# Performance work log

Measured on AMD Instinct MI355X. Metric: run time of the kernel, lower is better.

Reference implementation:

```python
import jax, jax.numpy as jnp
import numpy as np

T, N, E, D, H, L = 8, 50000, 800000, 128, 128, 2


def setup_inputs() -> dict:
    key = jax.random.key(0)
    ks = jax.random.split(key, 16)
    s = 1.0 / np.sqrt(H)  # glorot-ish scale so gates don't saturate
    inp = {
        "x": jax.random.normal(ks[0], (T, N, D), jnp.float32),
        "h0": jax.random.normal(ks[1], (L, N, H), jnp.float32) * 0.1,
        "edge_index": jax.random.randint(ks[2], (2, E), 0, N, jnp.int32),
    }
    for j, n in enumerate(["Wxz", "Whz", "Wxr", "Whr", "Wxh", "Whh"]):
        inp[n] = jax.random.normal(ks[3 + j], (L, H, H), jnp.float32) * s
    for n in ["bxz", "bhz", "bxr", "bhr", "bxh", "bhh"]:
        inp[n] = jnp.zeros((L, H), jnp.float32)
    return inp


def reference(x, h0, Wxz, Whz, Wxr, Whr, Wxh, Whh,
              bxz, bhz, bxr, bhr, bxh, bhh, edge_index):
    n_nodes = x.shape[1]
    n_layer = h0.shape[0]
    # GCNConv(improved=True): add self-loops with weight 2, symmetric norm.
    loop = jnp.arange(n_nodes, dtype=edge_index.dtype)
    row = jnp.concatenate([edge_index[0], loop])
    col = jnp.concatenate([edge_index[1], loop])
    w = jnp.concatenate([jnp.ones((edge_index.shape[1],), x.dtype),
                         jnp.full((n_nodes,), 2.0, x.dtype)])
    deg = jax.ops.segment_sum(w, row, num_segments=n_nodes)
    dinv = jnp.where(deg > 0, deg ** -0.5, 0.0)
    norm = dinv[row] * w * dinv[col]  # [E+N]

    def gcn(v, W, b):
        # gather -> weight -> scatter-add (identity activation inside GRU)
        m = norm[:, None] * (v @ W)[col]          # [E+N, H]
        return jax.ops.segment_sum(m, row, num_segments=n_nodes) + b

    def step(h, xt):
        hs = []
        inp = xt
        for i in range(n_layer):
            z = jax.nn.sigmoid(gcn(inp, Wxz[i], bxz[i]) + gcn(h[i], Whz[i], bhz[i]))
            r = jax.nn.sigmoid(gcn(inp, Wxr[i], bxr[i]) + gcn(h[i], Whr[i], bhr[i]))
            h_tilde = jnp.tanh(gcn(inp, Wxh[i], bxh[i]) + gcn(r * h[i], Whh[i], bhh[i]))
            hn = z * h[i] + (1.0 - z) * h_tilde
            hs.append(hn)
            inp = hn
        h_new = jnp.stack(hs)
        return h_new, h_new[-1]

    _, hs_top = jax.lax.scan(step, h0, x)  # [T, N, H] top-layer states
    return hs_top
```

## Files before the change

kernel.cpp:

```cpp
#include <hip/hip_runtime.h>
#include <hip/hip_fp16.h>

#define TT 8
#define NN 50000
#define EE 800000
#define HH 128
#define LL 2

typedef __attribute__((ext_vector_type(8))) short short8_t;
typedef __attribute__((ext_vector_type(4))) float f32x4;
typedef __attribute__((ext_vector_type(2))) float f32x2;

__device__ __forceinline__ float bf2f(unsigned short b){ return __uint_as_float(((unsigned)b)<<16); }
__device__ __forceinline__ unsigned short f2bf(float f){
  unsigned u = __float_as_uint(f);
  u += 0x7fffu + ((u>>16)&1u);
  return (unsigned short)(u>>16);
}
__device__ __forceinline__ float fin(float v){
  return (v == v && fabsf(v) < 1e30f) ? v : 0.0f;
}
__device__ __forceinline__ float sigm(float x){ return 1.0f/(1.0f+__expf(-x)); }
__device__ __forceinline__ float tanh_fast(float x){
  float t = __expf(-2.0f*fabsf(x));
  float r = (1.0f-t)/(1.0f+t);
  return copysignf(r,x);
}
__device__ __forceinline__ float2 up2(unsigned v){
  __half2 a = *(__half2*)&v;
  return __half22float2(a);
}
__device__ __forceinline__ unsigned packh2(float a, float b){
  __half2 h; h.x = __float2half_rn(a); h.y = __float2half_rn(b);
  return *(unsigned*)&h;
}
__device__ __forceinline__ float4 up4_fp8(unsigned v){
  f32x2 lo = __builtin_amdgcn_cvt_pk_f32_fp8(v, false);
  f32x2 hi = __builtin_amdgcn_cvt_pk_f32_fp8(v, true);
  return float4{lo[0], lo[1], hi[0], hi[1]};
}
__device__ __forceinline__ unsigned char f2fp8(float v){
  int w = __builtin_amdgcn_cvt_pk_fp8_f32(v, v, 0, false);
  return (unsigned char)(w & 0xFF);
}

__global__ void k_detect(const unsigned short* __restrict__ xr, int* __restrict__ flag){
  __shared__ int sm[256];
  int bad = 0;
  for (int i = threadIdx.x; i < 4096; i += 256){
    float v = bf2f(xr[i]);
    if (!(fabsf(v) < 64.0f)) bad++;
  }
  sm[threadIdx.x] = bad; __syncthreads();
  for (int off=128; off>0; off>>=1){
    if (threadIdx.x < off) sm[threadIdx.x] += sm[threadIdx.x+off];
    __syncthreads();
  }
  if (threadIdx.x == 0) flag[0] = (sm[0] > 8) ? 1 : 0;
}

__global__ void k_hist(const int* __restrict__ row, int* __restrict__ counts, int E){
  int e = blockIdx.x*256 + threadIdx.x;
  if (e < E){
    int r = row[e];
    if ((unsigned)r < (unsigned)NN) atomicAdd(&counts[r], 1);
  }
}
__global__ void k_dinv(const int* __restrict__ counts, float* __restrict__ dinv, int N){
  int i = blockIdx.x*256 + threadIdx.x;
  if (i < N) dinv[i] = rsqrtf((float)counts[i] + 2.0f);
}
__global__ void k_reduce(const int* __restrict__ counts, int* __restrict__ part, int N){
  __shared__ int sm[256];
  int i = blockIdx.x*256 + threadIdx.x;
  sm[threadIdx.x] = (i < N) ? counts[i] : 0;
  __syncthreads();
  for (int off=128; off>0; off>>=1){
    if (threadIdx.x < off) sm[threadIdx.x] += sm[threadIdx.x+off];
    __syncthreads();
  }
  if (threadIdx.x == 0) part[blockIdx.x] = sm[0];
}
__global__ void k_scan_partials(const int* __restrict__ part, int* __restrict__ pscan,
                                int nb, int* __restrict__ rowptr, int N, int E){
  __shared__ int sm[256];
  int t = threadIdx.x;
  int v = (t < nb) ? part[t] : 0;
  sm[t] = v; __syncthreads();
  for (int off=1; off<256; off<<=1){
    int x = (t >= off) ? sm[t-off] : 0;
    __syncthreads();
    sm[t] += x;
    __syncthreads();
  }
  if (t < nb) pscan[t] = sm[t] - v;
  if (t == 0) rowptr[N] = E;
}
__global__ void k_scan_final(const int* __restrict__ counts, const int* __restrict__ pscan,
                             int* __restrict__ rowptr, int* __restrict__ cursor, int N){
  __shared__ int sm[256];
  int t = threadIdx.x;
  int i = blockIdx.x*256 + t;
  int v = (i < N) ? counts[i] : 0;
  sm[t] = v; __syncthreads();
  for (int off=1; off<256; off<<=1){
    int x = (t >= off) ? sm[t-off] : 0;
    __syncthreads();
    sm[t] += x;
    __syncthreads();
  }
  int ex = sm[t] - v + pscan[blockIdx.x];
  if (i < N){ rowptr[i] = ex; cursor[i] = ex; }
}
__global__ void k_fill(const int* __restrict__ row, const int* __restrict__ col,
                       int* __restrict__ cursor, const float* __restrict__ dinv,
                       int2* __restrict__ ew, int E){
  int e = blockIdx.x*256 + threadIdx.x;
  if (e < E){
    int r = row[e];
    if ((unsigned)r >= (unsigned)NN) return;
    int p = atomicAdd(&cursor[r], 1);
    if ((unsigned)p >= (unsigned)EE) return;
    int c = col[e];
    if ((unsigned)c >= (unsigned)NN) c = 0;
    ew[p] = make_int2(c, __float_as_int(dinv[c]));
  }
}
__global__ void k_h0(const void* __restrict__ h0, float* __restrict__ h,
                     const int* __restrict__ flag, int n){
  const int fl = *flag;
  int i = blockIdx.x*256 + threadIdx.x;
  if (i < n){
    float v = fl ? ((const float*)h0)[i] : bf2f(((const unsigned short*)h0)[i]);
    h[i] = fin(v);
  }
}
__global__ void k_transpose(const void* W0, const void* W1, const void* W2,
                            const void* W3, const void* W4, const void* W5,
                            unsigned short* __restrict__ Wt_hi,
                            unsigned short* __restrict__ Wt_lo,
                            const int* __restrict__ flag){
  const int fl = *flag;
  int mat = blockIdx.y;
  int wsel = mat >> 1, l = mat & 1;
  const void* W;
  switch (wsel){
    case 0: W = W0; break; case 1: W = W1; break; case 2: W = W2; break;
    case 3: W = W3; break; case 4: W = W4; break; default: W = W5; break;
  }
  int idx = blockIdx.x*256 + threadIdx.x;
  int n = idx >> 7, k = idx & 127;
  size_t src = (size_t)l*16384 + (size_t)k*128 + n;
  float v = fl ? ((const float*)W)[src] : bf2f(((const unsigned short*)W)[src]);
  v = fin(v);
  unsigned short hi = f2bf(v);
  unsigned short lo = f2bf(v - bf2f(hi));
  Wt_hi[(size_t)mat*16384 + idx] = hi;
  Wt_lo[(size_t)mat*16384 + idx] = lo;
}

__global__ __launch_bounds__(256) void gemm_zr(
    const void* __restrict__ S1, long s1_off, int s1_is_x,
    const float* __restrict__ S2,
    const unsigned short* __restrict__ Wz0, const unsigned short* __restrict__ Wz1,
    const unsigned short* __restrict__ Wz2, const unsigned short* __restrict__ Wz3,
    const unsigned short* __restrict__ Wr0, const unsigned short* __restrict__ Wr1,
    const unsigned short* __restrict__ Wr2, const unsigned short* __restrict__ Wr3,
    unsigned char* __restrict__ Uzr8,
    int M, const int* __restrict__ flag)
{
  __shared__ short Alds[128*72];
  __shared__ short Bz[128*72];
  __shared__ short Br[128*72];
  const int fl = *flag;
  const int s1bf = s1_is_x && !fl;
  const int nit = fl ? 16 : 8;
  const int tid = threadIdx.x;
  const int m0 = blockIdx.x * 128;

  const int lane = tid & 63;
  const int wid  = tid >> 6;
  const int wm = (wid & 1) << 6;
  const int wn = (wid >> 1) << 6;
  const int lrow = lane & 15;
  const int lk   = (lane >> 4) << 3;

  f32x4 az[4][4], ar[4][4];
#pragma unroll
  for (int i=0;i<4;++i)
#pragma unroll
    for (int j=0;j<4;++j){ az[i][j] = f32x4{0.f,0.f,0.f,0.f}; ar[i][j] = f32x4{0.f,0.f,0.f,0.f}; }

  const int mrow = tid >> 1;
  const int hf   = tid & 1;
  int arow_g = m0 + mrow; if (arow_g >= M) arow_g = M-1;

  for (int it=0; it<nit; ++it){
    const int phase = it >> 2;
    const int k0 = (it & 3) * 32;
    const int koff = k0 + hf*16;
    const bool useS1 = (phase & 1) == 0;
    {
      unsigned pk[16];
      if (useS1 && s1bf){
        const unsigned short* sp = (const unsigned short*)S1 + s1_off + (size_t)arow_g*HH + koff;
        __align__(16) unsigned short tmp[16];
        *(uint4*)&tmp[0] = ((const uint4*)sp)[0];
        *(uint4*)&tmp[8] = ((const uint4*)sp)[1];
#pragma unroll
        for (int j=0;j<16;++j){
          unsigned short t = tmp[j];
          if ((t & 0x7F80u) == 0x7F80u) t = 0;
          pk[j] = (unsigned)t;
        }
      } else {
        __align__(16) float f[16];
        if (useS1){
          const float* sp = (const float*)S1 + s1_off + (size_t)arow_g*HH + koff;
          *(float4*)&f[0]  = ((const float4*)sp)[0];
          *(float4*)&f[4]  = ((const float4*)sp)[1];
          *(float4*)&f[8]  = ((const float4*)sp)[2];
          *(float4*)&f[12] = ((const float4*)sp)[3];
        } else {
          const float* sp = S2 + (size_t)arow_g*HH + koff;
          *(float4*)&f[0]  = ((const float4*)sp)[0];
          *(float4*)&f[4]  = ((const float4*)sp)[1];
          *(float4*)&f[8]  = ((const float4*)sp)[2];
          *(float4*)&f[12] = ((const float4*)sp)[3];
        }
#pragma unroll
        for (int j=0;j<16;++j){
          float v = fin(f[j]);
          unsigned short hi = f2bf(v);
          unsigned short lo = f2bf(v - bf2f(hi));
          pk[j] = (unsigned)hi | ((unsigned)lo << 16);
        }
      }
      short* arp = &Alds[mrow*72 + hf*32];
#pragma unroll
      for (int q=0;q<4;++q){
        uint4 v; v.x=pk[q*4+0]; v.y=pk[q*4+1]; v.z=pk[q*4+2]; v.w=pk[q*4+3];
        *(uint4*)(void*)(arp + q*8) = v;
      }
    }
    {
      const unsigned short* wz = (phase==0) ? Wz0 : (phase==1) ? Wz1 : (phase==2) ? Wz2 : Wz3;
      const unsigned short* wr = (phase==0) ? Wr0 : (phase==1) ? Wr1 : (phase==2) ? Wr2 : Wr3;
      const unsigned short* wpz = wz + (size_t)mrow*HH + koff;
      const unsigned short* wpr = wr + (size_t)mrow*HH + koff;
      __align__(16) unsigned short tz[16], tr[16];
      *(uint4*)&tz[0] = ((const uint4*)wpz)[0];
      *(uint4*)&tz[8] = ((const uint4*)wpz)[1];
      *(uint4*)&tr[0] = ((const uint4*)wpr)[0];
      *(uint4*)&tr[8] = ((const uint4*)wpr)[1];
      short* bzp = &Bz[mrow*72 + hf*32];
      short* brp = &Br[mrow*72 + hf*32];
#pragma unroll
      for (int q=0;q<4;++q){
        uint4 vz, vr;
        vz.x = ((unsigned)tz[q*4+0])*0x00010001u; vz.y = ((unsigned)tz[q*4+1])*0x00010001u;
        vz.z = ((unsigned)tz[q*4+2])*0x00010001u; vz.w = ((unsigned)tz[q*4+3])*0x00010001u;
        vr.x = ((unsigned)tr[q*4+0])*0x00010001u; vr.y = ((unsigned)tr[q*4+1])*0x00010001u;
        vr.z = ((unsigned)tr[q*4+2])*0x00010001u; vr.w = ((unsigned)tr[q*4+3])*0x00010001u;
        *(uint4*)(void*)(bzp + q*8) = vz;
        *(uint4*)(void*)(brp + q*8) = vr;
      }
    }
    __syncthreads();
#pragma unroll
    for (int ks=0; ks<2; ++ks){
      short8_t af[4], bz[4], br[4];
#pragma unroll
      for (int mt=0;mt<4;++mt)
        af[mt] = *(const short8_t*)&Alds[(wm + mt*16 + lrow)*72 + ks*32 + lk];
#pragma unroll
      for (int nt=0;nt<4;++nt){
        bz[nt] = *(const short8_t*)&Bz[(wn + nt*16 + lrow)*72 + ks*32 + lk];
        br[nt] = *(const short8_t*)&Br[(wn + nt*16 + lrow)*72 + ks*32 + lk];
      }
#pragma unroll
      for (int mt=0;mt<4;++mt)
#pragma unroll
        for (int nt=0;nt<4;++nt){
          az[mt][nt] = __builtin_amdgcn_mfma_f32_16x16x32_bf16(af[mt], bz[nt], az[mt][nt], 0, 0, 0);
          ar[mt][nt] = __builtin_amdgcn_mfma_f32_16x16x32_bf16(af[mt], br[nt], ar[mt][nt], 0, 0, 0);
        }
    }
    __syncthreads();
  }
#pragma unroll
  for (int mt=0;mt<4;++mt){
    int rbase = m0 + wm + mt*16 + ((lane>>4)<<2);
#pragma unroll
    for (int nt=0;nt<4;++nt){
      int cc = wn + nt*16 + (lane & 15);
      f32x4 vz = az[mt][nt];
      f32x4 vr = ar[mt][nt];
#pragma unroll
      for (int r=0;r<4;++r){
        int row = rbase + r;
        if (row < M){
          Uzr8[(size_t)row*256 + cc]       = f2fp8(vz[r]);
          Uzr8[(size_t)row*256 + 128 + cc] = f2fp8(vr[r]);
        }
      }
    }
  }
}

__global__ __launch_bounds__(256) void gemm_h(
    const void* __restrict__ S1, long s1_off, int s1_is_x,
    const __half* __restrict__ S2,
    const unsigned short* __restrict__ W0, const unsigned short* __restrict__ W1,
    const unsigned short* __restrict__ W2, const unsigned short* __restrict__ W3,
    __half* __restrict__ C, int M, const int* __restrict__ flag)
{
  __shared__ short Alds[128*72];
  __shared__ short Blds[128*72];
  const int fl = *flag;
  const int s1bf = s1_is_x && !fl;
  const int nit = fl ? 16 : 8;
  const int tid = threadIdx.x;
  const int m0 = blockIdx.x * 128;

  const int lane = tid & 63;
  const int wid  = tid >> 6;
  const int wm = (wid & 1) << 6;
  const int wn = (wid >> 1) << 6;
  const int lrow = lane & 15;
  const int lk   = (lane >> 4) << 3;

  f32x4 acc[4][4];
#pragma unroll
  for (int i=0;i<4;++i)
#pragma unroll
    for (int j=0;j<4;++j) acc[i][j] = f32x4{0.f,0.f,0.f,0.f};

  const int mrow = tid >> 1;
  const int hf = tid & 1;
  int arow_g = m0 + mrow; if (arow_g >= M) arow_g = M-1;

  for (int it=0; it<nit; ++it){
    const int phase = it >> 2;
    const int k0 = (it & 3) * 32;
    const int koff = k0 + hf*16;
    const bool useS1 = (phase & 1) == 0;
    {
      unsigned pk[16];
      if (useS1 && s1bf){
        const unsigned short* sp = (const unsigned short*)S1 + s1_off + (size_t)arow_g*HH + koff;
        __align__(16) unsigned short tmp[16];
        *(uint4*)&tmp[0] = ((const uint4*)sp)[0];
        *(uint4*)&tmp[8] = ((const uint4*)sp)[1];
#pragma unroll
        for (int j=0;j<16;++j){
          unsigned short t = tmp[j];
          if ((t & 0x7F80u) == 0x7F80u) t = 0;
          pk[j] = (unsigned)t;
        }
      } else {
        __align__(16) float f[16];
        if (useS1){
          const float* sp = (const float*)S1 + s1_off + (size_t)arow_g*HH + koff;
          *(float4*)&f[0]  = ((const float4*)sp)[0];
          *(float4*)&f[4]  = ((const float4*)sp)[1];
          *(float4*)&f[8]  = ((const float4*)sp)[2];
          *(float4*)&f[12] = ((const float4*)sp)[3];
        } else {
          const __half* sp = S2 + (size_t)arow_g*HH + koff;
          __align__(16) __half tmp[16];
          *(uint4*)&tmp[0] = ((const uint4*)sp)[0];
          *(uint4*)&tmp[8] = ((const uint4*)sp)[1];
#pragma unroll
          for (int j=0;j<16;++j) f[j] = __half2float(tmp[j]);
        }
#pragma unroll
        for (int j=0;j<16;++j){
          float v = fin(f[j]);
          unsigned short hi = f2bf(v);
          unsigned short lo = f2bf(v - bf2f(hi));
          pk[j] = (unsigned)hi | ((unsigned)lo << 16);
        }
      }
      short* arp = &Alds[mrow*72 + hf*32];
#pragma unroll
      for (int q=0;q<4;++q){
        uint4 v; v.x=pk[q*4+0]; v.y=pk[q*4+1]; v.z=pk[q*4+2]; v.w=pk[q*4+3];
        *(uint4*)(void*)(arp + q*8) = v;
      }
    }
    {
      const unsigned short* wb = (phase==0) ? W0 : (phase==1) ? W1 : (phase==2) ? W2 : W3;
      const unsigned short* wp = wb + (size_t)mrow*HH + koff;
      __align__(16) unsigned short tb[16];
      *(uint4*)&tb[0] = ((const uint4*)wp)[0];
      *(uint4*)&tb[8] = ((const uint4*)wp)[1];
      unsigned pb[16];
#pragma unroll
      for (int j=0;j<16;++j) pb[j] = ((unsigned)tb[j]) * 0x00010001u;
      short* brp = &Blds[mrow*72 + hf*32];
#pragma unroll
      for (int q=0;q<4;++q){
        uint4 v; v.x=pb[q*4+0]; v.y=pb[q*4+1]; v.z=pb[q*4+2]; v.w=pb[q*4+3];
        *(uint4*)(void*)(brp + q*8) = v;
      }
    }
    __syncthreads();
#pragma unroll
    for (int ks=0; ks<2; ++ks){
      short8_t af[4], bfr[4];
#pragma unroll
      for (int mt=0;mt<4;++mt)
        af[mt] = *(const short8_t*)&Alds[(wm + mt*16 + lrow)*72 + ks*32 + lk];
#pragma unroll
      for (int nt=0;nt<4;++nt)
        bfr[nt] = *(const short8_t*)&Blds[(wn + nt*16 + lrow)*72 + ks*32 + lk];
#pragma unroll
      for (int mt=0;mt<4;++mt)
#pragma unroll
        for (int nt=0;nt<4;++nt)
          acc[mt][nt] = __builtin_amdgcn_mfma_f32_16x16x32_bf16(af[mt], bfr[nt], acc[mt][nt], 0, 0, 0);
    }
    __syncthreads();
  }
#pragma unroll
  for (int mt=0;mt<4;++mt){
    int rbase = m0 + wm + mt*16 + ((lane>>4)<<2);
#pragma unroll
    for (int nt=0;nt<4;++nt){
      int cc = wn + nt*16 + (lane & 15);
      f32x4 a = acc[mt][nt];
#pragma unroll
      for (int r=0;r<4;++r){
        int row = rbase + r;
        if (row < M) C[(size_t)row*HH + cc] = __float2half_rn(a[r]);
      }
    }
  }
}

__global__ __launch_bounds__(256) void prop_zr(
    const unsigned char* __restrict__ Uzr8,
    const int* __restrict__ rowptr, const int2* __restrict__ ew,
    const float* __restrict__ dinv,
    const void* __restrict__ bxz, const void* __restrict__ bhz,
    const void* __restrict__ bxr, const void* __restrict__ bhr, int boff,
    const float* __restrict__ hl, __half2* __restrict__ zbuf,
    __half2* __restrict__ rhbuf, const int* __restrict__ flag, int N)
{
  const int fl = *flag;
  int lane = threadIdx.x & 63;
  int d = (blockIdx.x << 2) + (threadIdx.x >> 6);
  if (d >= N) return;
  float di = dinv[d];
  const unsigned* U1 = (const unsigned*)Uzr8;
  unsigned sv = U1[(size_t)d*64 + lane];
  float4 sf = up4_fp8(sv);
  float sw = 2.0f*di;
  float4 a = float4{sw*sf.x, sw*sf.y, sw*sf.z, sw*sf.w};
  int b = rowptr[d], e = rowptr[d+1];
  if (b < 0) b = 0; if (e > EE) e = EE; if (e < b) e = b;
  for (int base=b; base<e; base+=64){
    int cnt = e - base; if (cnt > 64) cnt = 64;
    int idx = base + lane;
    int2 ev = (idx < e) ? ew[idx] : make_int2(0,0);
    int mc = ev.x; float mw = __int_as_float(ev.y);
    if ((unsigned)mc >= (unsigned)NN){ mc = 0; mw = 0.0f; }
    int j = 0;
    for (; j+7 < cnt; j += 8){
      int s0 = __shfl(mc, j),   s1 = __shfl(mc, j+1);
      int s2 = __shfl(mc, j+2), s3 = __shfl(mc, j+3);
      int s4 = __shfl(mc, j+4), s5 = __shfl(mc, j+5);
      int s6 = __shfl(mc, j+6), s7 = __shfl(mc, j+7);
      float w0 = __shfl(mw, j),   w1 = __shfl(mw, j+1);
      float w2 = __shfl(mw, j+2), w3 = __shfl(mw, j+3);
      float w4 = __shfl(mw, j+4), w5 = __shfl(mw, j+5);
      float w6 = __shfl(mw, j+6), w7 = __shfl(mw, j+7);
      unsigned v0 = U1[(size_t)s0*64 + lane];
      unsigned v1 = U1[(size_t)s1*64 + lane];
      unsigned v2 = U1[(size_t)s2*64 + lane];
      unsigned v3 = U1[(size_t)s3*64 + lane];
      unsigned v4 = U1[(size_t)s4*64 + lane];
      unsigned v5 = U1[(size_t)s5*64 + lane];
      unsigned v6 = U1[(size_t)s6*64 + lane];
      unsigned v7 = U1[(size_t)s7*64 + lane];
      float4 g0 = up4_fp8(v0), g1 = up4_fp8(v1), g2 = up4_fp8(v2), g3 = up4_fp8(v3);
      float4 g4 = up4_fp8(v4), g5 = up4_fp8(v5), g6 = up4_fp8(v6), g7 = up4_fp8(v7);
      a.x += w0*g0.x; a.y += w0*g0.y; a.z += w0*g0.z; a.w += w0*g0.w;
      a.x += w1*g1.x; a.y += w1*g1.y; a.z += w1*g1.z; a.w += w1*g1.w;
      a.x += w2*g2.x; a.y += w2*g2.y; a.z += w2*g2.z; a.w += w2*g2.w;
      a.x += w3*g3.x; a.y += w3*g3.y; a.z += w3*g3.z; a.w += w3*g3.w;
      a.x += w4*g4.x; a.y += w4*g4.y; a.z += w4*g4.z; a.w += w4*g4.w;
      a.x += w5*g5.x; a.y += w5*g5.y; a.z += w5*g5.z; a.w += w5*g5.w;
      a.x += w6*g6.x; a.y += w6*g6.y; a.z += w6*g6.z; a.w += w6*g6.w;
      a.x += w7*g7.x; a.y += w7*g7.y; a.z += w7*g7.z; a.w += w7*g7.w;
    }
    for (; j < cnt; ++j){
      int s = __shfl(mc, j);
      float w = __shfl(mw, j);
      float4 g = up4_fp8(U1[(size_t)s*64 + lane]);
      a.x += w*g.x; a.y += w*g.y; a.z += w*g.z; a.w += w*g.w;
    }
  }
  int l5 = lane & 31;
  int c = boff + (l5 << 2);
  if (lane < 32){
    float bz0 = fl ? ((const float*)bxz)[c+0] : bf2f(((const unsigned short*)bxz)[c+0]);
    float bz1 = fl ? ((const float*)bxz)[c+1] : bf2f(((const unsigned short*)bxz)[c+1]);
    float bz2 = fl ? ((const float*)bxz)[c+2] : bf2f(((const unsigned short*)bxz)[c+2]);
    float bz3 = fl ? ((const float*)bxz)[c+3] : bf2f(((const unsigned short*)bxz)[c+3]);
    float hz0 = fl ? ((const float*)bhz)[c+0] : bf2f(((const unsigned short*)bhz)[c+0]);
    float hz1 = fl ? ((const float*)bhz)[c+1] : bf2f(((const unsigned short*)bhz)[c+1]);
    float hz2 = fl ? ((const float*)bhz)[c+2] : bf2f(((const unsigned short*)bhz)[c+2]);
    float hz3 = fl ? ((const float*)bhz)[c+3] : bf2f(((const unsigned short*)bhz)[c+3]);
    float g0 = sigm(di*a.x + fin(bz0) + fin(hz0));
    float g1 = sigm(di*a.y + fin(bz1) + fin(hz1));
    float g2 = sigm(di*a.z + fin(bz2) + fin(hz2));
    float g3 = sigm(di*a.w + fin(bz3) + fin(hz3));
    uint2 o; o.x = packh2(g0, g1); o.y = packh2(g2, g3);
    ((uint2*)zbuf)[(size_t)d*32 + l5] = o;
  } else {
    float br0 = fl ? ((const float*)bxr)[c+0] : bf2f(((const unsigned short*)bxr)[c+0]);
    float br1 = fl ? ((const float*)bxr)[c+1] : bf2f(((const unsigned short*)bxr)[c+1]);
    float br2 = fl ? ((const float*)bxr)[c+2] : bf2f(((const unsigned short*)bxr)[c+2]);
    float br3 = fl ? ((const float*)bxr)[c+3] : bf2f(((const unsigned short*)bxr)[c+3]);
    float hr0 = fl ? ((const float*)bhr)[c+0] : bf2f(((const unsigned short*)bhr)[c+0]);
    float hr1 = fl ? ((const float*)bhr)[c+1] : bf2f(((const unsigned short*)bhr)[c+1]);
    float hr2 = fl ? ((const float*)bhr)[c+2] : bf2f(((const unsigned short*)bhr)[c+2]);
    float hr3 = fl ? ((const float*)bhr)[c+3] : bf2f(((const unsigned short*)bhr)[c+3]);
    float r0 = sigm(di*a.x + fin(br0) + fin(hr0));
    float r1 = sigm(di*a.y + fin(br1) + fin(hr1));
    float r2 = sigm(di*a.z + fin(br2) + fin(hr2));
    float r3 = sigm(di*a.w + fin(br3) + fin(hr3));
    float4 hv = ((const float4*)hl)[(size_t)d*32 + l5];
    uint2 o; o.x = packh2(r0*hv.x, r1*hv.y); o.y = packh2(r2*hv.z, r3*hv.w);
    ((uint2*)rhbuf)[(size_t)d*32 + l5] = o;
  }
}

__global__ __launch_bounds__(256) void prop_h(
    const __half* __restrict__ U, const int* __restrict__ rowptr,
    const int2* __restrict__ ew, const float* __restrict__ dinv,
    const void* __restrict__ bx, const void* __restrict__ bh, int boff,
    const __half2* __restrict__ zbuf, float* __restrict__ hl,
    void* __restrict__ outbase, long out_off, int has_out,
    const int* __restrict__ flag, int N)
{
  const int fl = *flag;
  int lane = threadIdx.x & 63;
  int d = (blockIdx.x << 2) + (threadIdx.x >> 6);
  if (d >= N) return;
  float di = dinv[d];
  const unsigned* U1 = (const unsigned*)U;
  float2 sf = up2(U1[(size_t)d*64 + lane]);
  float sw = 2.0f*di;
  float2 a = float2{sw*sf.x, sw*sf.y};
  int b = rowptr[d], e = rowptr[d+1];
  if (b < 0) b = 0; if (e > EE) e = EE; if (e < b) e = b;
  for (int base=b; base<e; base+=64){
    int cnt = e - base; if (cnt > 64) cnt = 64;
    int idx = base + lane;
    int2 ev = (idx < e) ? ew[idx] : make_int2(0,0);
    int mc = ev.x; float mw = __int_as_float(ev.y);
    if ((unsigned)mc >= (unsigned)NN){ mc = 0; mw = 0.0f; }
    int j = 0;
    for (; j+7 < cnt; j += 8){
      int s0 = __shfl(mc, j),   s1 = __shfl(mc, j+1);
      int s2 = __shfl(mc, j+2), s3 = __shfl(mc, j+3);
      int s4 = __shfl(mc, j+4), s5 = __shfl(mc, j+5);
      int s6 = __shfl(mc, j+6), s7 = __shfl(mc, j+7);
      float w0 = __shfl(mw, j),   w1 = __shfl(mw, j+1);
      float w2 = __shfl(mw, j+2), w3 = __shfl(mw, j+3);
      float w4 = __shfl(mw, j+4), w5 = __shfl(mw, j+5);
      float w6 = __shfl(mw, j+6), w7 = __shfl(mw, j+7);
      unsigned v0 = U1[(size_t)s0*64 + lane];
      unsigned v1 = U1[(size_t)s1*64 + lane];
      unsigned v2 = U1[(size_t)s2*64 + lane];
      unsigned v3 = U1[(size_t)s3*64 + lane];
      unsigned v4 = U1[(size_t)s4*64 + lane];
      unsigned v5 = U1[(size_t)s5*64 + lane];
      unsigned v6 = U1[(size_t)s6*64 + lane];
      unsigned v7 = U1[(size_t)s7*64 + lane];
      float2 g0 = up2(v0), g1 = up2(v1), g2 = up2(v2), g3 = up2(v3);
      float2 g4 = up2(v4), g5 = up2(v5), g6 = up2(v6), g7 = up2(v7);
      a.x += w0*g0.x; a.y += w0*g0.y;
      a.x += w1*g1.x; a.y += w1*g1.y;
      a.x += w2*g2.x; a.y += w2*g2.y;
      a.x += w3*g3.x; a.y += w3*g3.y;
      a.x += w4*g4.x; a.y += w4*g4.y;
      a.x += w5*g5.x; a.y += w5*g5.y;
      a.x += w6*g6.x; a.y += w6*g6.y;
      a.x += w7*g7.x; a.y += w7*g7.y;
    }
    for (; j < cnt; ++j){
      int s = __shfl(mc, j);
      float w = __shfl(mw, j);
      float2 g = up2(U1[(size_t)s*64 + lane]);
      a.x += w*g.x; a.y += w*g.y;
    }
  }
  int c = boff + (lane << 1);
  float bx0 = fl ? ((const float*)bx)[c]   : bf2f(((const unsigned short*)bx)[c]);
  float bx1 = fl ? ((const float*)bx)[c+1] : bf2f(((const unsigned short*)bx)[c+1]);
  float bh0 = fl ? ((const float*)bh)[c]   : bf2f(((const unsigned short*)bh)[c]);
  float bh1 = fl ? ((const float*)bh)[c+1] : bf2f(((const unsigned short*)bh)[c+1]);
  float ht0 = tanh_fast(di*a.x + fin(bx0) + fin(bh0));
  float ht1 = tanh_fast(di*a.y + fin(bx1) + fin(bh1));
  __half2 zv2 = zbuf[(size_t)d*64 + lane];
  float z0 = __half2float(zv2.x), z1 = __half2float(zv2.y);
  float2 hv = ((const float2*)hl)[(size_t)d*64 + lane];
  float hn0 = z0*hv.x + (1.0f - z0)*ht0;
  float hn1 = z1*hv.y + (1.0f - z1)*ht1;
  ((float2*)hl)[(size_t)d*64 + lane] = float2{hn0, hn1};
  if (has_out){
    if (fl){
      float* op = (float*)outbase + out_off;
      ((float2*)op)[(size_t)d*64 + lane] = float2{hn0, hn1};
    } else {
      unsigned short* op = (unsigned short*)outbase + out_off;
      ((unsigned int*)op)[(size_t)d*64 + lane] =
          (unsigned)f2bf(hn0) | ((unsigned)f2bf(hn1) << 16);
    }
  }
}

extern "C" void kernel_launch(void* const* d_in, const int* in_sizes, int n_in,
                              void* d_out, int out_size, void* d_ws, size_t ws_size,
                              hipStream_t stream)
{
  const void* x  = d_in[0];
  const void* h0 = d_in[1];
  const int* ei  = (const int*)d_in[2];
  const void* Wm[6] = { d_in[3], d_in[4], d_in[5], d_in[6], d_in[7], d_in[8] };
  const void* bxz = d_in[9];
  const void* bhz = d_in[10];
  const void* bxr = d_in[11];
  const void* bhr = d_in[12];
  const void* bxh = d_in[13];
  const void* bhh = d_in[14];

  char* wp_ = (char*)d_ws;
  auto alloc = [&](size_t b)->char*{ char* p = wp_; wp_ += (b + 255) & ~(size_t)255; return p; };
  int*   flag  = (int*)alloc(256);
  float* dinv  = (float*)alloc((size_t)NN*4);
  int*   counts= (int*)alloc((size_t)NN*4);
  int*   rowptr= (int*)alloc((size_t)(NN+1)*4);
  int*   cursor= (int*)alloc((size_t)NN*4);
  int*   part  = (int*)alloc(1024);
  int*   pscan = (int*)alloc(1024);
  int2*  ew    = (int2*)alloc((size_t)EE*8);
  unsigned short* Wt_hi = (unsigned short*)alloc((size_t)12*16384*2);
  unsigned short* Wt_lo = (unsigned short*)alloc((size_t)12*16384*2);
  float*   h     = (float*)alloc((size_t)LL*NN*HH*4);
  unsigned char* Uzr8 = (unsigned char*)alloc((size_t)NN*256);
  __half*  Uh    = (__half*)alloc((size_t)NN*HH*2);
  __half2* zbuf  = (__half2*)alloc((size_t)NN*HH*2);
  __half2* rhbuf = (__half2*)alloc((size_t)NN*HH*2);

  k_detect<<<1, 256, 0, stream>>>((const unsigned short*)x, flag);
  hipMemsetAsync(counts, 0, (size_t)NN*4, stream);
  hipMemsetAsync(ew, 0, (size_t)EE*8, stream);
  k_hist<<<(EE+255)/256, 256, 0, stream>>>(ei, counts, EE);
  k_dinv<<<(NN+255)/256, 256, 0, stream>>>(counts, dinv, NN);
  k_reduce<<<196, 256, 0, stream>>>(counts, part, NN);
  k_scan_partials<<<1, 256, 0, stream>>>(part, pscan, 196, rowptr, NN, EE);
  k_scan_final<<<196, 256, 0, stream>>>(counts, pscan, rowptr, cursor, NN);
  k_fill<<<(EE+255)/256, 256, 0, stream>>>(ei, ei+EE, cursor, dinv, ew, EE);
  k_h0<<<(LL*NN*HH+255)/256, 256, 0, stream>>>(h0, h, flag, LL*NN*HH);
  k_transpose<<<dim3(64,12), 256, 0, stream>>>(Wm[0],Wm[1],Wm[2],Wm[3],Wm[4],Wm[5],
                                               Wt_hi, Wt_lo, flag);

  const int gx = (NN + 127) / 128;
  const int pg = NN / 4;
  for (int t=0; t<TT; ++t){
    for (int l=0; l<LL; ++l){
      const void* S1 = (l==0) ? x : (const void*)h;
      long s1_off = (l==0) ? (long)t*NN*HH : 0;
      int s1_is_x = (l==0) ? 1 : 0;
      float* hl = h + (size_t)l*NN*HH;
      gemm_zr<<<gx, 256, 0, stream>>>(S1, s1_off, s1_is_x, hl,
          Wt_hi + (0*2+l)*16384, Wt_hi + (1*2+l)*16384,
          Wt_lo + (0*2+l)*16384, Wt_lo + (1*2+l)*16384,
          Wt_hi + (2*2+l)*16384, Wt_hi + (3*2+l)*16384,
          Wt_lo + (2*2+l)*16384, Wt_lo + (3*2+l)*16384,
          Uzr8, NN, flag);
      prop_zr<<<pg, 256, 0, stream>>>(Uzr8, rowptr, ew, dinv,
          bxz, bhz, bxr, bhr, l*HH, hl, zbuf, rhbuf, flag, NN);
      gemm_h<<<gx, 256, 0, stream>>>(S1, s1_off, s1_is_x, (const __half*)rhbuf,
          Wt_hi + (4*2+l)*16384, Wt_hi + (5*2+l)*16384,
          Wt_lo + (4*2+l)*16384, Wt_lo + (5*2+l)*16384, Uh, NN, flag);
      prop_h<<<pg, 256, 0, stream>>>(Uh, rowptr, ew, dinv,
          bxh, bhh, l*HH, zbuf, hl,
          d_out, (long)t*NN*HH, (l==LL-1) ? 1 : 0, flag, NN);
    }
  }
}
```

Baseline: 3.526 ms.

## Load GEMM weights directly into registers and use half-wave-per-node propagation

The GEMM kernels stop staging the weight (B) tiles through shared memory. Each lane now reads its bf16 weight fragment straight from global memory (L2-resident) and expands it into the hi/lo MFMA layout in registers, which halves or thirds the LDS footprint and removes the LDS write/read traffic for B. The propagation kernels switch from one 64-lane wave per destination node to one 32-lane half-wave per node with 8-byte gathers, so each wave handles two nodes and each lane issues wider loads. The trade-offs are more global-load latency inside the MFMA loop and half as many neighbours gathered in parallel per node.

```diff
diff --git a/kernel.cpp b/kernel.cpp
--- a/kernel.cpp
+++ b/kernel.cpp
@@ -170,8 +170,6 @@
     int M, const int* __restrict__ flag)
 {
   __shared__ short Alds[128*72];
-  __shared__ short Bz[128*72];
-  __shared__ short Br[128*72];
   const int fl = *flag;
   const int s1bf = s1_is_x && !fl;
   const int nit = fl ? 16 : 8;
@@ -243,48 +241,35 @@
         *(uint4*)(void*)(arp + q*8) = v;
       }
     }
-    {
-      const unsigned short* wz = (phase==0) ? Wz0 : (phase==1) ? Wz1 : (phase==2) ? Wz2 : Wz3;
-      const unsigned short* wr = (phase==0) ? Wr0 : (phase==1) ? Wr1 : (phase==2) ? Wr2 : Wr3;
-      const unsigned short* wpz = wz + (size_t)mrow*HH + koff;
-      const unsigned short* wpr = wr + (size_t)mrow*HH + koff;
-      __align__(16) unsigned short tz[16], tr[16];
-      *(uint4*)&tz[0] = ((const uint4*)wpz)[0];
-      *(uint4*)&tz[8] = ((const uint4*)wpz)[1];
-      *(uint4*)&tr[0] = ((const uint4*)wpr)[0];
-      *(uint4*)&tr[8] = ((const uint4*)wpr)[1];
-      short* bzp = &Bz[mrow*72 + hf*32];
-      short* brp = &Br[mrow*72 + hf*32];
-#pragma unroll
-      for (int q=0;q<4;++q){
-        uint4 vz, vr;
-        vz.x = ((unsigned)tz[q*4+0])*0x00010001u; vz.y = ((unsigned)tz[q*4+1])*0x00010001u;
-        vz.z = ((unsigned)tz[q*4+2])*0x00010001u; vz.w = ((unsigned)tz[q*4+3])*0x00010001u;
-        vr.x = ((unsigned)tr[q*4+0])*0x00010001u; vr.y = ((unsigned)tr[q*4+1])*0x00010001u;
-        vr.z = ((unsigned)tr[q*4+2])*0x00010001u; vr.w = ((unsigned)tr[q*4+3])*0x00010001u;
-        *(uint4*)(void*)(bzp + q*8) = vz;
-        *(uint4*)(void*)(brp + q*8) = vr;
-      }
-    }
+    const unsigned short* wzp = (phase==0) ? Wz0 : (phase==1) ? Wz1 : (phase==2) ? Wz2 : Wz3;
+    const unsigned short* wrp = (phase==0) ? Wr0 : (phase==1) ? Wr1 : (phase==2) ? Wr2 : Wr3;
     __syncthreads();
 #pragma unroll
     for (int ks=0; ks<2; ++ks){
-      short8_t af[4], bz[4], br[4];
+      short8_t af[4];
 #pragma unroll
       for (int mt=0;mt<4;++mt)
         af[mt] = *(const short8_t*)&Alds[(wm + mt*16 + lrow)*72 + ks*32 + lk];
+      const int kcol = k0 + ks*16 + ((lane>>4)<<2);
 #pragma unroll
       for (int nt=0;nt<4;++nt){
-        bz[nt] = *(const short8_t*)&Bz[(wn + nt*16 + lrow)*72 + ks*32 + lk];
-        br[nt] = *(const short8_t*)&Br[(wn + nt*16 + lrow)*72 + ks*32 + lk];
-      }
-#pragma unroll
-      for (int mt=0;mt<4;++mt)
-#pragma unroll
-        for (int nt=0;nt<4;++nt){
-          az[mt][nt] = __builtin_amdgcn_mfma_f32_16x16x32_bf16(af[mt], bz[nt], az[mt][nt], 0, 0, 0);
-          ar[mt][nt] = __builtin_amdgcn_mfma_f32_16x16x32_bf16(af[mt], br[nt], ar[mt][nt], 0, 0, 0);
-        }
+        const int nrow = wn + nt*16 + lrow;
+        uint2 wzv = *(const uint2*)(wzp + (size_t)nrow*HH + kcol);
+        uint2 wrv = *(const uint2*)(wrp + (size_t)nrow*HH + kcol);
+        __align__(16) unsigned bz_[4];
+        __align__(16) unsigned br_[4];
+        bz_[0]=(wzv.x & 0xFFFFu)*0x00010001u; bz_[1]=(wzv.x>>16)*0x00010001u;
+        bz_[2]=(wzv.y & 0xFFFFu)*0x00010001u; bz_[3]=(wzv.y>>16)*0x00010001u;
+        br_[0]=(wrv.x & 0xFFFFu)*0x00010001u; br_[1]=(wrv.x>>16)*0x00010001u;
+        br_[2]=(wrv.y & 0xFFFFu)*0x00010001u; br_[3]=(wrv.y>>16)*0x00010001u;
+        short8_t bzf = *(const short8_t*)bz_;
+        short8_t brf = *(const short8_t*)br_;
+#pragma unroll
+        for (int mt=0;mt<4;++mt){
+          az[mt][nt] = __builtin_amdgcn_mfma_f32_16x16x32_bf16(af[mt], bzf, az[mt][nt], 0, 0, 0);
+          ar[mt][nt] = __builtin_amdgcn_mfma_f32_16x16x32_bf16(af[mt], brf, ar[mt][nt], 0, 0, 0);
+        }
+      }
     }
     __syncthreads();
   }
@@ -316,7 +301,6 @@
     __half* __restrict__ C, int M, const int* __restrict__ flag)
 {
   __shared__ short Alds[128*72];
-  __shared__ short Blds[128*72];
   const int fl = *flag;
   const int s1bf = s1_is_x && !fl;
   const int nit = fl ? 16 : 8;
@@ -389,37 +373,27 @@
         *(uint4*)(void*)(arp + q*8) = v;
       }
     }
-    {
-      const unsigned short* wb = (phase==0) ? W0 : (phase==1) ? W1 : (phase==2) ? W2 : W3;
-      const unsigned short* wp = wb + (size_t)mrow*HH + koff;
-      __align__(16) unsigned short tb[16];
-      *(uint4*)&tb[0] = ((const uint4*)wp)[0];
-      *(uint4*)&tb[8] = ((const uint4*)wp)[1];
-      unsigned pb[16];
-#pragma unroll
-      for (int j=0;j<16;++j) pb[j] = ((unsigned)tb[j]) * 0x00010001u;
-      short* brp = &Blds[mrow*72 + hf*32];
-#pragma unroll
-      for (int q=0;q<4;++q){
-        uint4 v; v.x=pb[q*4+0]; v.y=pb[q*4+1]; v.z=pb[q*4+2]; v.w=pb[q*4+3];
-        *(uint4*)(void*)(brp + q*8) = v;
-      }
-    }
+    const unsigned short* wbp = (phase==0) ? W0 : (phase==1) ? W1 : (phase==2) ? W2 : W3;
     __syncthreads();
 #pragma unroll
     for (int ks=0; ks<2; ++ks){
-      short8_t af[4], bfr[4];
+      short8_t af[4];
 #pragma unroll
       for (int mt=0;mt<4;++mt)
         af[mt] = *(const short8_t*)&Alds[(wm + mt*16 + lrow)*72 + ks*32 + lk];
-#pragma unroll
-      for (int nt=0;nt<4;++nt)
-        bfr[nt] = *(const short8_t*)&Blds[(wn + nt*16 + lrow)*72 + ks*32 + lk];
-#pragma unroll
-      for (int mt=0;mt<4;++mt)
-#pragma unroll
-        for (int nt=0;nt<4;++nt)
-          acc[mt][nt] = __builtin_amdgcn_mfma_f32_16x16x32_bf16(af[mt], bfr[nt], acc[mt][nt], 0, 0, 0);
+      const int kcol = k0 + ks*16 + ((lane>>4)<<2);
+#pragma unroll
+      for (int nt=0;nt<4;++nt){
+        const int nrow = wn + nt*16 + lrow;
+        uint2 wv = *(const uint2*)(wbp + (size_t)nrow*HH + kcol);
+        __align__(16) unsigned bb_[4];
+        bb_[0]=(wv.x & 0xFFFFu)*0x00010001u; bb_[1]=(wv.x>>16)*0x00010001u;
+        bb_[2]=(wv.y & 0xFFFFu)*0x00010001u; bb_[3]=(wv.y>>16)*0x00010001u;
+        short8_t bf_ = *(const short8_t*)bb_;
+#pragma unroll
+        for (int mt=0;mt<4;++mt)
+          acc[mt][nt] = __builtin_amdgcn_mfma_f32_16x16x32_bf16(af[mt], bf_, acc[mt][nt], 0, 0, 0);
+      }
     }
     __syncthreads();
   }
@@ -450,91 +424,87 @@
 {
   const int fl = *flag;
   int lane = threadIdx.x & 63;
-  int d = (blockIdx.x << 2) + (threadIdx.x >> 6);
+  int l5 = lane & 31;
+  int d = (blockIdx.x << 3) + ((threadIdx.x >> 6) << 1) + (lane >> 5);
   if (d >= N) return;
   float di = dinv[d];
-  const unsigned* U1 = (const unsigned*)Uzr8;
-  unsigned sv = U1[(size_t)d*64 + lane];
-  float4 sf = up4_fp8(sv);
+  const uint2* U2 = (const uint2*)Uzr8;
+  uint2 sv = U2[(size_t)d*32 + l5];
+  float4 s0f = up4_fp8(sv.x), s1f = up4_fp8(sv.y);
   float sw = 2.0f*di;
-  float4 a = float4{sw*sf.x, sw*sf.y, sw*sf.z, sw*sf.w};
+  float4 aA = float4{sw*s0f.x, sw*s0f.y, sw*s0f.z, sw*s0f.w};
+  float4 aB = float4{sw*s1f.x, sw*s1f.y, sw*s1f.z, sw*s1f.w};
   int b = rowptr[d], e = rowptr[d+1];
   if (b < 0) b = 0; if (e > EE) e = EE; if (e < b) e = b;
-  for (int base=b; base<e; base+=64){
-    int cnt = e - base; if (cnt > 64) cnt = 64;
-    int idx = base + lane;
+  for (int base=b; base<e; base+=32){
+    int cnt = e - base; if (cnt > 32) cnt = 32;
+    int idx = base + l5;
     int2 ev = (idx < e) ? ew[idx] : make_int2(0,0);
     int mc = ev.x; float mw = __int_as_float(ev.y);
     if ((unsigned)mc >= (unsigned)NN){ mc = 0; mw = 0.0f; }
     int j = 0;
     for (; j+7 < cnt; j += 8){
-      int s0 = __shfl(mc, j),   s1 = __shfl(mc, j+1);
-      int s2 = __shfl(mc, j+2), s3 = __shfl(mc, j+3);
-      int s4 = __shfl(mc, j+4), s5 = __shfl(mc, j+5);
-      int s6 = __shfl(mc, j+6), s7 = __shfl(mc, j+7);
-      float w0 = __shfl(mw, j),   w1 = __shfl(mw, j+1);
-      float w2 = __shfl(mw, j+2), w3 = __shfl(mw, j+3);
-      float w4 = __shfl(mw, j+4), w5 = __shfl(mw, j+5);
-      float w6 = __shfl(mw, j+6), w7 = __shfl(mw, j+7);
-      unsigned v0 = U1[(size_t)s0*64 + lane];
-      unsigned v1 = U1[(size_t)s1*64 + lane];
-      unsigned v2 = U1[(size_t)s2*64 + lane];
-      unsigned v3 = U1[(size_t)s3*64 + lane];
-      unsigned v4 = U1[(size_t)s4*64 + lane];
-      unsigned v5 = U1[(size_t)s5*64 + lane];
-      unsigned v6 = U1[(size_t)s6*64 + lane];
-      unsigned v7 = U1[(size_t)s7*64 + lane];
-      float4 g0 = up4_fp8(v0), g1 = up4_fp8(v1), g2 = up4_fp8(v2), g3 = up4_fp8(v3);
-      float4 g4 = up4_fp8(v4), g5 = up4_fp8(v5), g6 = up4_fp8(v6), g7 = up4_fp8(v7);
-      a.x += w0*g0.x; a.y += w0*g0.y; a.z += w0*g0.z; a.w += w0*g0.w;
-      a.x += w1*g1.x; a.y += w1*g1.y; a.z += w1*g1.z; a.w += w1*g1.w;
-      a.x += w2*g2.x; a.y += w2*g2.y; a.z += w2*g2.z; a.w += w2*g2.w;
-      a.x += w3*g3.x; a.y += w3*g3.y; a.z += w3*g3.z; a.w += w3*g3.w;
-      a.x += w4*g4.x; a.y += w4*g4.y; a.z += w4*g4.z; a.w += w4*g4.w;
-      a.x += w5*g5.x; a.y += w5*g5.y; a.z += w5*g5.z; a.w += w5*g5.w;
-      a.x += w6*g6.x; a.y += w6*g6.y; a.z += w6*g6.z; a.w += w6*g6.w;
-      a.x += w7*g7.x; a.y += w7*g7.y; a.z += w7*g7.z; a.w += w7*g7.w;
+      int s0 = __shfl(mc, j,   32), s1 = __shfl(mc, j+1, 32);
+      int s2 = __shfl(mc, j+2, 32), s3 = __shfl(mc, j+3, 32);
+      int s4 = __shfl(mc, j+4, 32), s5 = __shfl(mc, j+5, 32);
+      int s6 = __shfl(mc, j+6, 32), s7 = __shfl(mc, j+7, 32);
+      float w0 = __shfl(mw, j,   32), w1 = __shfl(mw, j+1, 32);
+      float w2 = __shfl(mw, j+2, 32), w3 = __shfl(mw, j+3, 32);
+      float w4 = __shfl(mw, j+4, 32), w5 = __shfl(mw, j+5, 32);
+      float w6 = __shfl(mw, j+6, 32), w7 = __shfl(mw, j+7, 32);
+      uint2 v0 = U2[(size_t)s0*32 + l5];
+      uint2 v1 = U2[(size_t)s1*32 + l5];
+      uint2 v2 = U2[(size_t)s2*32 + l5];
+      uint2 v3 = U2[(size_t)s3*32 + l5];
+      uint2 v4 = U2[(size_t)s4*32 + l5];
+      uint2 v5 = U2[(size_t)s5*32 + l5];
+      uint2 v6 = U2[(size_t)s6*32 + l5];
+      uint2 v7 = U2[(size_t)s7*32 + l5];
+#define ACC_ZR(vv, ww) { float4 gA = up4_fp8(vv.x), gB = up4_fp8(vv.y); \
+      aA.x += ww*gA.x; aA.y += ww*gA.y; aA.z += ww*gA.z; aA.w += ww*gA.w; \
+      aB.x += ww*gB.x; aB.y += ww*gB.y; aB.z += ww*gB.z; aB.w += ww*gB.w; }
+      ACC_ZR(v0, w0) ACC_ZR(v1, w1) ACC_ZR(v2, w2) ACC_ZR(v3, w3)
+      ACC_ZR(v4, w4) ACC_ZR(v5, w5) ACC_ZR(v6, w6) ACC_ZR(v7, w7)
     }
     for (; j < cnt; ++j){
-      int s = __shfl(mc, j);
-      float w = __shfl(mw, j);
-      float4 g = up4_fp8(U1[(size_t)s*64 + lane]);
-      a.x += w*g.x; a.y += w*g.y; a.z += w*g.z; a.w += w*g.w;
-    }
-  }
-  int l5 = lane & 31;
-  int c = boff + (l5 << 2);
-  if (lane < 32){
-    float bz0 = fl ? ((const float*)bxz)[c+0] : bf2f(((const unsigned short*)bxz)[c+0]);
-    float bz1 = fl ? ((const float*)bxz)[c+1] : bf2f(((const unsigned short*)bxz)[c+1]);
-    float bz2 = fl ? ((const float*)bxz)[c+2] : bf2f(((const unsigned short*)bxz)[c+2]);
-    float bz3 = fl ? ((const float*)bxz)[c+3] : bf2f(((const unsigned short*)bxz)[c+3]);
-    float hz0 = fl ? ((const float*)bhz)[c+0] : bf2f(((const unsigned short*)bhz)[c+0]);
-    float hz1 = fl ? ((const float*)bhz)[c+1] : bf2f(((const unsigned short*)bhz)[c+1]);
-    float hz2 = fl ? ((const float*)bhz)[c+2] : bf2f(((const unsigned short*)bhz)[c+2]);
-    float hz3 = fl ? ((const float*)bhz)[c+3] : bf2f(((const unsigned short*)bhz)[c+3]);
-    float g0 = sigm(di*a.x + fin(bz0) + fin(hz0));
-    float g1 = sigm(di*a.y + fin(bz1) + fin(hz1));
-    float g2 = sigm(di*a.z + fin(bz2) + fin(hz2));
-    float g3 = sigm(di*a.w + fin(bz3) + fin(hz3));
-    uint2 o; o.x = packh2(g0, g1); o.y = packh2(g2, g3);
-    ((uint2*)zbuf)[(size_t)d*32 + l5] = o;
+      int s = __shfl(mc, j, 32);
+      float w = __shfl(mw, j, 32);
+      uint2 v = U2[(size_t)s*32 + l5];
+      ACC_ZR(v, w)
+    }
+#undef ACC_ZR
+  }
+  float av[8] = {aA.x, aA.y, aA.z, aA.w, aB.x, aB.y, aB.z, aB.w};
+  if (l5 < 16){
+    int c0 = boff + (l5 << 3);
+    float g[8];
+#pragma unroll
+    for (int i=0;i<8;++i){
+      float b1 = fl ? ((const float*)bxz)[c0+i] : bf2f(((const unsigned short*)bxz)[c0+i]);
+      float b2 = fl ? ((const float*)bhz)[c0+i] : bf2f(((const unsigned short*)bhz)[c0+i]);
+      g[i] = sigm(di*av[i] + fin(b1) + fin(b2));
+    }
+    uint4 o; o.x = packh2(g[0],g[1]); o.y = packh2(g[2],g[3]);
+    o.z = packh2(g[4],g[5]); o.w = packh2(g[6],g[7]);
+    ((uint4*)zbuf)[(size_t)d*16 + l5] = o;
   } else {
-    float br0 = fl ? ((const float*)bxr)[c+0] : bf2f(((const unsigned short*)bxr)[c+0]);
-    float br1 = fl ? ((const float*)bxr)[c+1] : bf2f(((const unsigned short*)bxr)[c+1]);
-    float br2 = fl ? ((const float*)bxr)[c+2] : bf2f(((const unsigned short*)bxr)[c+2]);
-    float br3 = fl ? ((const float*)bxr)[c+3] : bf2f(((const unsigned short*)bxr)[c+3]);
-    float hr0 = fl ? ((const float*)bhr)[c+0] : bf2f(((const unsigned short*)bhr)[c+0]);
-    float hr1 = fl ? ((const float*)bhr)[c+1] : bf2f(((const unsigned short*)bhr)[c+1]);
-    float hr2 = fl ? ((const float*)bhr)[c+2] : bf2f(((const unsigned short*)bhr)[c+2]);
-    float hr3 = fl ? ((const float*)bhr)[c+3] : bf2f(((const unsigned short*)bhr)[c+3]);
-    float r0 = sigm(di*a.x + fin(br0) + fin(hr0));
-    float r1 = sigm(di*a.y + fin(br1) + fin(hr1));
-    float r2 = sigm(di*a.z + fin(br2) + fin(hr2));
-    float r3 = sigm(di*a.w + fin(br3) + fin(hr3));
-    float4 hv = ((const float4*)hl)[(size_t)d*32 + l5];
-    uint2 o; o.x = packh2(r0*hv.x, r1*hv.y); o.y = packh2(r2*hv.z, r3*hv.w);
-    ((uint2*)rhbuf)[(size_t)d*32 + l5] = o;
+    int q = l5 - 16;
+    int c0 = boff + (q << 3);
+    float g[8];
+#pragma unroll
+    for (int i=0;i<8;++i){
+      float b1 = fl ? ((const float*)bxr)[c0+i] : bf2f(((const unsigned short*)bxr)[c0+i]);
+      float b2 = fl ? ((const float*)bhr)[c0+i] : bf2f(((const unsigned short*)bhr)[c0+i]);
+      g[i] = sigm(di*av[i] + fin(b1) + fin(b2));
+    }
+    float4 hv0 = ((const float4*)hl)[(size_t)d*32 + 2*q];
+    float4 hv1 = ((const float4*)hl)[(size_t)d*32 + 2*q + 1];
+    uint4 o;
+    o.x = packh2(g[0]*hv0.x, g[1]*hv0.y);
+    o.y = packh2(g[2]*hv0.z, g[3]*hv0.w);
+    o.z = packh2(g[4]*hv1.x, g[5]*hv1.y);
+    o.w = packh2(g[6]*hv1.z, g[7]*hv1.w);
+    ((uint4*)rhbuf)[(size_t)d*16 + q] = o;
   }
 }
 
@@ -548,78 +518,80 @@
 {
   const int fl = *flag;
   int lane = threadIdx.x & 63;
-  int d = (blockIdx.x << 2) + (threadIdx.x >> 6);
+  int l5 = lane & 31;
+  int d = (blockIdx.x << 3) + ((threadIdx.x >> 6) << 1) + (lane >> 5);
   if (d >= N) return;
   float di = dinv[d];
-  const unsigned* U1 = (const unsigned*)U;
-  float2 sf = up2(U1[(size_t)d*64 + lane]);
+  const uint2* U2 = (const uint2*)U;
+  uint2 sv = U2[(size_t)d*32 + l5];
+  float2 s0f = up2(sv.x), s1f = up2(sv.y);
   float sw = 2.0f*di;
-  float2 a = float2{sw*sf.x, sw*sf.y};
+  float4 a = float4{sw*s0f.x, sw*s0f.y, sw*s1f.x, sw*s1f.y};
   int b = rowptr[d], e = rowptr[d+1];
   if (b < 0) b = 0; if (e > EE) e = EE; if (e < b) e = b;
-  for (int base=b; base<e; base+=64){
-    int cnt = e - base; if (cnt > 64) cnt = 64;
-    int idx = base + lane;
+  for (int base=b; base<e; base+=32){
+    int cnt = e - base; if (cnt > 32) cnt = 32;
+    int idx = base + l5;
     int2 ev = (idx < e) ? ew[idx] : make_int2(0,0);
     int mc = ev.x; float mw = __int_as_float(ev.y);
     if ((unsigned)mc >= (unsigned)NN){ mc = 0; mw = 0.0f; }
     int j = 0;
     for (; j+7 < cnt; j += 8){
-      int s0 = __shfl(mc, j),   s1 = __shfl(mc, j+1);
-      int s2 = __shfl(mc, j+2), s3 = __shfl(mc, j+3);
-      int s4 = __shfl(mc, j+4), s5 = __shfl(mc, j+5);
-      int s6 = __shfl(mc, j+6), s7 = __shfl(mc, j+7);
-      float w0 = __shfl(mw, j),   w1 = __shfl(mw, j+1);
-      float w2 = __shfl(mw, j+2), w3 = __shfl(mw, j+3);
-      float w4 = __shfl(mw, j+4), w5 = __shfl(mw, j+5);
-      float w6 = __shfl(mw, j+6), w7 = __shfl(mw, j+7);
-      unsigned v0 = U1[(size_t)s0*64 + lane];
-      unsigned v1 = U1[(size_t)s1*64 + lane];
-      unsigned v2 = U1[(size_t)s2*64 + lane];
-      unsigned v3 = U1[(size_t)s3*64 + lane];
-      unsigned v4 = U1[(size_t)s4*64 + lane];
-      unsigned v5 = U1[(size_t)s5*64 + lane];
-      unsigned v6 = U1[(size_t)s6*64 + lane];
-      unsigned v7 = U1[(size_t)s7*64 + lane];
-      float2 g0 = up2(v0), g1 = up2(v1), g2 = up2(v2), g3 = up2(v3);
-      float2 g4 = up2(v4), g5 = up2(v5), g6 = up2(v6), g7 = up2(v7);
-      a.x += w0*g0.x; a.y += w0*g0.y;
-      a.x += w1*g1.x; a.y += w1*g1.y;
-      a.x += w2*g2.x; a.y += w2*g2.y;
-      a.x += w3*g3.x; a.y += w3*g3.y;
-      a.x += w4*g4.x; a.y += w4*g4.y;
-      a.x += w5*g5.x; a.y += w5*g5.y;
-      a.x += w6*g6.x; a.y += w6*g6.y;
-      a.x += w7*g7.x; a.y += w7*g7.y;
+      int s0 = __shfl(mc, j,   32), s1 = __shfl(mc, j+1, 32);
+      int s2 = __shfl(mc, j+2, 32), s3 = __shfl(mc, j+3, 32);
+      int s4 = __shfl(mc, j+4, 32), s5 = __shfl(mc, j+5, 32);
+      int s6 = __shfl(mc, j+6, 32), s7 = __shfl(mc, j+7, 32);
+      float w0 = __shfl(mw, j,   32), w1 = __shfl(mw, j+1, 32);
+      float w2 = __shfl(mw, j+2, 32), w3 = __shfl(mw, j+3, 32);
+      float w4 = __shfl(mw, j+4, 32), w5 = __shfl(mw, j+5, 32);
+      float w6 = __shfl(mw, j+6, 32), w7 = __shfl(mw, j+7, 32);
+      uint2 v0 = U2[(size_t)s0*32 + l5];
+      uint2 v1 = U2[(size_t)s1*32 + l5];
+      uint2 v2 = U2[(size_t)s2*32 + l5];
+      uint2 v3 = U2[(size_t)s3*32 + l5];
+      uint2 v4 = U2[(size_t)s4*32 + l5];
+      uint2 v5 = U2[(size_t)s5*32 + l5];
+      uint2 v6 = U2[(size_t)s6*32 + l5];
+      uint2 v7 = U2[(size_t)s7*32 + l5];
+#define ACC_H(vv, ww) { float2 gx = up2(vv.x), gy = up2(vv.y); \
+      a.x += ww*gx.x; a.y += ww*gx.y; a.z += ww*gy.x; a.w += ww*gy.y; }
+      ACC_H(v0, w0) ACC_H(v1, w1) ACC_H(v2, w2) ACC_H(v3, w3)
+      ACC_H(v4, w4) ACC_H(v5, w5) ACC_H(v6, w6) ACC_H(v7, w7)
     }
     for (; j < cnt; ++j){
-      int s = __shfl(mc, j);
-      float w = __shfl(mw, j);
-      float2 g = up2(U1[(size_t)s*64 + lane]);
-      a.x += w*g.x; a.y += w*g.y;
-    }
-  }
-  int c = boff + (lane << 1);
-  float bx0 = fl ? ((const float*)bx)[c]   : bf2f(((const unsigned short*)bx)[c]);
-  float bx1 = fl ? ((const float*)bx)[c+1] : bf2f(((const unsigned short*)bx)[c+1]);
-  float bh0 = fl ? ((const float*)bh)[c]   : bf2f(((const unsigned short*)bh)[c]);
-  float bh1 = fl ? ((const float*)bh)[c+1] : bf2f(((const unsigned short*)bh)[c+1]);
-  float ht0 = tanh_fast(di*a.x + fin(bx0) + fin(bh0));
-  float ht1 = tanh_fast(di*a.y + fin(bx1) + fin(bh1));
-  __half2 zv2 = zbuf[(size_t)d*64 + lane];
-  float z0 = __half2float(zv2.x), z1 = __half2float(zv2.y);
-  float2 hv = ((const float2*)hl)[(size_t)d*64 + lane];
-  float hn0 = z0*hv.x + (1.0f - z0)*ht0;
-  float hn1 = z1*hv.y + (1.0f - z1)*ht1;
-  ((float2*)hl)[(size_t)d*64 + lane] = float2{hn0, hn1};
+      int s = __shfl(mc, j, 32);
+      float w = __shfl(mw, j, 32);
+      uint2 v = U2[(size_t)s*32 + l5];
+      ACC_H(v, w)
+    }
+#undef ACC_H
+  }
+  int c0 = boff + (l5 << 2);
+  float ht[4]; float av[4] = {a.x, a.y, a.z, a.w};
+#pragma unroll
+  for (int i=0;i<4;++i){
+    float b1 = fl ? ((const float*)bx)[c0+i] : bf2f(((const unsigned short*)bx)[c0+i]);
+    float b2 = fl ? ((const float*)bh)[c0+i] : bf2f(((const unsigned short*)bh)[c0+i]);
+    ht[i] = tanh_fast(di*av[i] + fin(b1) + fin(b2));
+  }
+  uint2 zv = ((const uint2*)zbuf)[(size_t)d*32 + l5];
+  float2 z01 = up2(zv.x), z23 = up2(zv.y);
+  float4 hv = ((const float4*)hl)[(size_t)d*32 + l5];
+  float hn0 = z01.x*hv.x + (1.0f - z01.x)*ht[0];
+  float hn1 = z01.y*hv.y + (1.0f - z01.y)*ht[1];
+  float hn2 = z23.x*hv.z + (1.0f - z23.x)*ht[2];
+  float hn3 = z23.y*hv.w + (1.0f - z23.y)*ht[3];
+  ((float4*)hl)[(size_t)d*32 + l5] = float4{hn0, hn1, hn2, hn3};
   if (has_out){
     if (fl){
       float* op = (float*)outbase + out_off;
-      ((float2*)op)[(size_t)d*64 + lane] = float2{hn0, hn1};
+      ((float4*)op)[(size_t)d*32 + l5] = float4{hn0, hn1, hn2, hn3};
     } else {
       unsigned short* op = (unsigned short*)outbase + out_off;
-      ((unsigned int*)op)[(size_t)d*64 + lane] =
-          (unsigned)f2bf(hn0) | ((unsigned)f2bf(hn1) << 16);
+      uint2 o;
+      o.x = (unsigned)f2bf(hn0) | ((unsigned)f2bf(hn1) << 16);
+      o.y = (unsigned)f2bf(hn2) | ((unsigned)f2bf(hn3) << 16);
+      ((uint2*)op)[(size_t)d*32 + l5] = o;
     }
   }
 }
@@ -671,7 +643,7 @@
                                                Wt_hi, Wt_lo, flag);
 
   const int gx = (NN + 127) / 128;
-  const int pg = NN / 4;
+  const int pg = NN / 8;
   for (int t=0; t<TT; ++t){
     for (int l=0; l<LL; ++l){
       const void* S1 = (l==0) ? x : (const void*)h;
```

Measured after the change: 4.738 ms. 34.4% more time.
